# Performance work log

Measured on AMD Instinct MI355X. Metric: run time of the kernel, lower is better.

Reference implementation:

```python
import jax, jax.numpy as jnp
import numpy as np


def setup_inputs() -> dict:
    key = jax.random.key(0)
    x = jax.random.normal(key, (16, 3, 512, 512), dtype=jnp.float32)
    return {"x": x}


def reference(x):
    # x: [B, C, H, W] with H, W even.
    B, C, H, W = x.shape
    # --- single-level 2D Haar DWT (pywt 'haar' convention) ---
    # View each 2x2 block: a=top-left, b=top-right, c=bottom-left, d=bottom-right.
    blocks = x.reshape(B, C, H // 2, 2, W // 2, 2)
    a = blocks[:, :, :, 0, :, 0]
    b = blocks[:, :, :, 0, :, 1]
    c = blocks[:, :, :, 1, :, 0]
    d = blocks[:, :, :, 1, :, 1]
    half = jnp.asarray(0.5, x.dtype)
    LL = (a + b + c + d) * half  # cA
    LH = (a + b - c - d) * half  # cH (horizontal detail)
    HL = (a - b + c - d) * half  # cV (vertical detail)
    HH = (a - b - c + d) * half  # cD (diagonal detail)
    # [B, C, 4, H/2, W/2]
    sub = jnp.stack([LL, LH, HL, HH], axis=2)
    # Bilinear upsample back to (H, W); jax.image bilinear uses half-pixel
    # centers, matching F.interpolate(mode='bilinear', align_corners=False).
    up = jax.image.resize(sub, (B, C, 4, H, W), method="bilinear")
    # IG: original channel resized to its own size -> identity under this mode.
    bands = jnp.concatenate([x[:, :, None], up], axis=2)  # [B, C, 5, H, W]
    return bands.reshape(B, 5 * C, H, W)
```

## Files before the change

kernel.cpp:

```cpp
#include <hip/hip_runtime.h>

#define HF   512
#define WF   512
#define HH   256
#define HW   (HF * WF)
#define TK   4

typedef float v4 __attribute__((ext_vector_type(4)));
typedef float v2 __attribute__((ext_vector_type(2)));

__device__ __forceinline__ v4 haar2(float a, float b, float c, float d) {
    const float s1 = a + b, d1 = a - b, s2 = c + d, d2 = c - d;
    v4 v;
    v.x = (s1 + s2) * 0.5f;
    v.y = (s1 - s2) * 0.5f;
    v.z = (d1 + d2) * 0.5f;
    v.w = (d1 - d2) * 0.5f;
    return v;
}

__device__ __forceinline__ void unit_compute(const float* __restrict__ p0,
                                             const float* __restrict__ p1,
                                             const float* __restrict__ p2,
                                             int x0, int xl, int xr,
                                             v4 (&ve)[4], v4 (&vo)[4]) {
    {
        const v2 lt = *reinterpret_cast<const v2*>(p0 + xl);
        const v2 lb = *reinterpret_cast<const v2*>(p0 + WF + xl);
        const v4 t  = *reinterpret_cast<const v4*>(p0 + x0);
        const v4 u  = *reinterpret_cast<const v4*>(p0 + WF + x0);
        const v2 rt = *reinterpret_cast<const v2*>(p0 + xr);
        const v2 rb = *reinterpret_cast<const v2*>(p0 + WF + xr);
        const v4 A = haar2(lt.x, lt.y, lb.x, lb.y);
        const v4 B = haar2(t.x,  t.y,  u.x,  u.y);
        const v4 C = haar2(t.z,  t.w,  u.z,  u.w);
        const v4 D = haar2(rt.x, rt.y, rb.x, rb.y);
        ve[0] = (A * 0.25f + B * 0.75f) * 0.25f;
        ve[1] = (B * 0.75f + C * 0.25f) * 0.25f;
        ve[2] = (B * 0.25f + C * 0.75f) * 0.25f;
        ve[3] = (C * 0.75f + D * 0.25f) * 0.25f;
    }
    {
        const v2 lt = *reinterpret_cast<const v2*>(p1 + xl);
        const v2 lb = *reinterpret_cast<const v2*>(p1 + WF + xl);
        const v4 t  = *reinterpret_cast<const v4*>(p1 + x0);
        const v4 u  = *reinterpret_cast<const v4*>(p1 + WF + x0);
        const v2 rt = *reinterpret_cast<const v2*>(p1 + xr);
        const v2 rb = *reinterpret_cast<const v2*>(p1 + WF + xr);
        const v4 A = haar2(lt.x, lt.y, lb.x, lb.y);
        const v4 B = haar2(t.x,  t.y,  u.x,  u.y);
        const v4 C = haar2(t.z,  t.w,  u.z,  u.w);
        const v4 D = haar2(rt.x, rt.y, rb.x, rb.y);
        v4 h;
        h = A * 0.25f + B * 0.75f;  ve[0] += h * 0.75f;  vo[0] = h * 0.75f;
        h = B * 0.75f + C * 0.25f;  ve[1] += h * 0.75f;  vo[1] = h * 0.75f;
        h = B * 0.25f + C * 0.75f;  ve[2] += h * 0.75f;  vo[2] = h * 0.75f;
        h = C * 0.75f + D * 0.25f;  ve[3] += h * 0.75f;  vo[3] = h * 0.75f;
    }
    {
        const v2 lt = *reinterpret_cast<const v2*>(p2 + xl);
        const v2 lb = *reinterpret_cast<const v2*>(p2 + WF + xl);
        const v4 t  = *reinterpret_cast<const v4*>(p2 + x0);
        const v4 u  = *reinterpret_cast<const v4*>(p2 + WF + x0);
        const v2 rt = *reinterpret_cast<const v2*>(p2 + xr);
        const v2 rb = *reinterpret_cast<const v2*>(p2 + WF + xr);
        const v4 A = haar2(lt.x, lt.y, lb.x, lb.y);
        const v4 B = haar2(t.x,  t.y,  u.x,  u.y);
        const v4 C = haar2(t.z,  t.w,  u.z,  u.w);
        const v4 D = haar2(rt.x, rt.y, rb.x, rb.y);
        vo[0] += (A * 0.25f + B * 0.75f) * 0.25f;
        vo[1] += (B * 0.75f + C * 0.25f) * 0.25f;
        vo[2] += (B * 0.25f + C * 0.75f) * 0.25f;
        vo[3] += (C * 0.75f + D * 0.25f) * 0.25f;
    }
}

__global__ __launch_bounds__(256) void wavelet_kernel(const float* __restrict__ x,
                                                      float* __restrict__ out) {
    const int tx = threadIdx.x;
    const int ty = threadIdx.y;
    const int k  = blockIdx.x * TK + ty;
    const int bc = blockIdx.y;

    const float* __restrict__ xin  = x   + (size_t)bc * HW;
    float*       __restrict__ outp = out + (size_t)bc * (size_t)(5 * HW);

    const int ku = (k == 0) ? 0 : k - 1;
    const int kd = (k == HH - 1) ? HH - 1 : k + 1;
    const float* p0 = xin + (size_t)(2 * ku) * WF;
    const float* p1 = xin + (size_t)(2 * k)  * WF;
    const float* p2 = xin + (size_t)(2 * kd) * WF;

    const int xA  = 4 * tx;
    const int xlA = (tx == 0) ? 0 : xA - 2;
    const int xrA = xA + 4;
    v4 veA[4], voA[4];
    unit_compute(p0, p1, p2, xA, xlA, xrA, veA, voA);

    const int xB  = 256 + 4 * tx;
    const int xlB = xB - 2;
    const int xrB = (tx == 63) ? (WF - 2) : (xB + 4);
    v4 veB[4], voB[4];
    unit_compute(p0, p1, p2, xB, xlB, xrB, veB, voB);

    const int y0 = 2 * k;

    {
        const v4 a0 = *reinterpret_cast<const v4*>(p1 + xA);
        const v4 b0 = *reinterpret_cast<const v4*>(p1 + xB);
        const v4 a1 = *reinterpret_cast<const v4*>(p1 + WF + xA);
        const v4 b1 = *reinterpret_cast<const v4*>(p1 + WF + xB);
        float* o = outp + (size_t)y0 * WF;
        __builtin_nontemporal_store(a0, reinterpret_cast<v4*>(o + xA));
        __builtin_nontemporal_store(b0, reinterpret_cast<v4*>(o + xB));
        __builtin_nontemporal_store(a1, reinterpret_cast<v4*>(o + WF + xA));
        __builtin_nontemporal_store(b1, reinterpret_cast<v4*>(o + WF + xB));
    }

#define STORE_BAND(BIDX, COMP)                                                         \
    {                                                                                  \
        v4 eA, eB, oA, oB;                                                             \
        eA.x = veA[0].COMP; eA.y = veA[1].COMP; eA.z = veA[2].COMP; eA.w = veA[3].COMP;\
        eB.x = veB[0].COMP; eB.y = veB[1].COMP; eB.z = veB[2].COMP; eB.w = veB[3].COMP;\
        oA.x = voA[0].COMP; oA.y = voA[1].COMP; oA.z = voA[2].COMP; oA.w = voA[3].COMP;\
        oB.x = voB[0].COMP; oB.y = voB[1].COMP; oB.z = voB[2].COMP; oB.w = voB[3].COMP;\
        float* o = outp + (size_t)BIDX * HW + (size_t)y0 * WF;                         \
        __builtin_nontemporal_store(eA, reinterpret_cast<v4*>(o + xA));                \
        __builtin_nontemporal_store(eB, reinterpret_cast<v4*>(o + xB));                \
        __builtin_nontemporal_store(oA, reinterpret_cast<v4*>(o + WF + xA));           \
        __builtin_nontemporal_store(oB, reinterpret_cast<v4*>(o + WF + xB));           \
    }
    STORE_BAND(1, x)
    STORE_BAND(2, y)
    STORE_BAND(3, z)
    STORE_BAND(4, w)
#undef STORE_BAND
}

extern "C" void kernel_launch(void* const* d_in, const int* in_sizes, int n_in,
                              void* d_out, int out_size, void* d_ws, size_t ws_size,
                              hipStream_t stream) {
    const float* x = (const float*)d_in[0];
    float* out = (float*)d_out;
    dim3 grid(HH / TK, 48);
    dim3 block(64, TK);
    hipLaunchKernelGGL(wavelet_kernel, grid, block, 0, stream, x, out);
}
```

Baseline: 283.4 us.

## Use persistent grid-stride waves, each writing one output band row-pair

Replaces the per-input-row-pair work split with a persistent grid of 1536 blocks. Each wave loops over (output plane, row-pair) units and writes a single band, so output writes walk sequentially through each plane instead of scattering across five planes. The price is redundant arithmetic and input loads: every detail band recomputes the full Haar/bilinear stencil and reads the three input row-pairs again. It also adds a data-dependent switch on the band index.

```diff
diff --git a/kernel.cpp b/kernel.cpp
--- a/kernel.cpp
+++ b/kernel.cpp
@@ -4,7 +4,10 @@
 #define WF   512
 #define HH   256
 #define HW   (HF * WF)
-#define TK   4
+#define NPLANES 240
+#define NUNITS  (NPLANES * HH)
+#define NBLK    1536
+#define NWAVES  (NBLK * 4)
 
 typedef float v4 __attribute__((ext_vector_type(4)));
 typedef float v2 __attribute__((ext_vector_type(2)));
@@ -77,64 +80,67 @@
 
 __global__ __launch_bounds__(256) void wavelet_kernel(const float* __restrict__ x,
                                                       float* __restrict__ out) {
-    const int tx = threadIdx.x;
-    const int ty = threadIdx.y;
-    const int k  = blockIdx.x * TK + ty;
-    const int bc = blockIdx.y;
-
-    const float* __restrict__ xin  = x   + (size_t)bc * HW;
-    float*       __restrict__ outp = out + (size_t)bc * (size_t)(5 * HW);
-
-    const int ku = (k == 0) ? 0 : k - 1;
-    const int kd = (k == HH - 1) ? HH - 1 : k + 1;
-    const float* p0 = xin + (size_t)(2 * ku) * WF;
-    const float* p1 = xin + (size_t)(2 * k)  * WF;
-    const float* p2 = xin + (size_t)(2 * kd) * WF;
+    const int tx  = threadIdx.x;
+    const int wid = blockIdx.x * 4 + threadIdx.y;
 
     const int xA  = 4 * tx;
     const int xlA = (tx == 0) ? 0 : xA - 2;
     const int xrA = xA + 4;
-    v4 veA[4], voA[4];
-    unit_compute(p0, p1, p2, xA, xlA, xrA, veA, voA);
-
     const int xB  = 256 + 4 * tx;
     const int xlB = xB - 2;
     const int xrB = (tx == 63) ? (WF - 2) : (xB + 4);
-    v4 veB[4], voB[4];
-    unit_compute(p0, p1, p2, xB, xlB, xrB, veB, voB);
 
-    const int y0 = 2 * k;
+    for (int u = wid; u < NUNITS; u += NWAVES) {
+        const int plane = u >> 8;
+        const int k     = u & (HH - 1);
+        const int bc    = plane / 5;
+        const int band  = plane - bc * 5;
 
-    {
-        const v4 a0 = *reinterpret_cast<const v4*>(p1 + xA);
-        const v4 b0 = *reinterpret_cast<const v4*>(p1 + xB);
-        const v4 a1 = *reinterpret_cast<const v4*>(p1 + WF + xA);
-        const v4 b1 = *reinterpret_cast<const v4*>(p1 + WF + xB);
-        float* o = outp + (size_t)y0 * WF;
-        __builtin_nontemporal_store(a0, reinterpret_cast<v4*>(o + xA));
-        __builtin_nontemporal_store(b0, reinterpret_cast<v4*>(o + xB));
-        __builtin_nontemporal_store(a1, reinterpret_cast<v4*>(o + WF + xA));
-        __builtin_nontemporal_store(b1, reinterpret_cast<v4*>(o + WF + xB));
+        const float* __restrict__ xin = x + (size_t)bc * HW;
+        float* __restrict__ orow = out + (size_t)plane * HW + (size_t)(2 * k) * WF;
+
+        if (band == 0) {
+            const float* p = xin + (size_t)(2 * k) * WF;
+            const v4 a0 = *reinterpret_cast<const v4*>(p + xA);
+            const v4 b0 = *reinterpret_cast<const v4*>(p + xB);
+            const v4 a1 = *reinterpret_cast<const v4*>(p + WF + xA);
+            const v4 b1 = *reinterpret_cast<const v4*>(p + WF + xB);
+            __builtin_nontemporal_store(a0, reinterpret_cast<v4*>(orow + xA));
+            __builtin_nontemporal_store(b0, reinterpret_cast<v4*>(orow + xB));
+            __builtin_nontemporal_store(a1, reinterpret_cast<v4*>(orow + WF + xA));
+            __builtin_nontemporal_store(b1, reinterpret_cast<v4*>(orow + WF + xB));
+        } else {
+            const int ku = (k == 0) ? 0 : k - 1;
+            const int kd = (k == HH - 1) ? HH - 1 : k + 1;
+            const float* p0 = xin + (size_t)(2 * ku) * WF;
+            const float* p1 = xin + (size_t)(2 * k)  * WF;
+            const float* p2 = xin + (size_t)(2 * kd) * WF;
+
+            v4 ve[4], vo[4];
+
+#define EXTRACT_STORE(COMP, XOFF)                                                      \
+            {                                                                          \
+                v4 e, o;                                                               \
+                e.x = ve[0].COMP; e.y = ve[1].COMP; e.z = ve[2].COMP; e.w = ve[3].COMP;\
+                o.x = vo[0].COMP; o.y = vo[1].COMP; o.z = vo[2].COMP; o.w = vo[3].COMP;\
+                __builtin_nontemporal_store(e, reinterpret_cast<v4*>(orow + (XOFF)));  \
+                __builtin_nontemporal_store(o, reinterpret_cast<v4*>(orow + WF + (XOFF)));\
+            }
+#define DO_UNIT(X0, XL, XR)                                                            \
+            unit_compute(p0, p1, p2, (X0), (XL), (XR), ve, vo);                        \
+            switch (band) {                                                            \
+                case 1: EXTRACT_STORE(x, X0) break;                                    \
+                case 2: EXTRACT_STORE(y, X0) break;                                    \
+                case 3: EXTRACT_STORE(z, X0) break;                                    \
+                default: EXTRACT_STORE(w, X0) break;                                   \
+            }
+
+            DO_UNIT(xA, xlA, xrA)
+            DO_UNIT(xB, xlB, xrB)
+#undef DO_UNIT
+#undef EXTRACT_STORE
+        }
     }
-
-#define STORE_BAND(BIDX, COMP)                                                         \
-    {                                                                                  \
-        v4 eA, eB, oA, oB;                                                             \
-        eA.x = veA[0].COMP; eA.y = veA[1].COMP; eA.z = veA[2].COMP; eA.w = veA[3].COMP;\
-        eB.x = veB[0].COMP; eB.y = veB[1].COMP; eB.z = veB[2].COMP; eB.w = veB[3].COMP;\
-        oA.x = voA[0].COMP; oA.y = voA[1].COMP; oA.z = voA[2].COMP; oA.w = voA[3].COMP;\
-        oB.x = voB[0].COMP; oB.y = voB[1].COMP; oB.z = voB[2].COMP; oB.w = voB[3].COMP;\
-        float* o = outp + (size_t)BIDX * HW + (size_t)y0 * WF;                         \
-        __builtin_nontemporal_store(eA, reinterpret_cast<v4*>(o + xA));                \
-        __builtin_nontemporal_store(eB, reinterpret_cast<v4*>(o + xB));                \
-        __builtin_nontemporal_store(oA, reinterpret_cast<v4*>(o + WF + xA));           \
-        __builtin_nontemporal_store(oB, reinterpret_cast<v4*>(o + WF + xB));           \
-    }
-    STORE_BAND(1, x)
-    STORE_BAND(2, y)
-    STORE_BAND(3, z)
-    STORE_BAND(4, w)
-#undef STORE_BAND
 }
 
 extern "C" void kernel_launch(void* const* d_in, const int* in_sizes, int n_in,
@@ -142,7 +148,7 @@
                               hipStream_t stream) {
     const float* x = (const float*)d_in[0];
     float* out = (float*)d_out;
-    dim3 grid(HH / TK, 48);
-    dim3 block(64, TK);
+    dim3 grid(NBLK);
+    dim3 block(64, 4);
     hipLaunchKernelGGL(wavelet_kernel, grid, block, 0, stream, x, out);
 }
```

Measured after the change: 329.3 us. 1.16x slower.
